# Performance work log

Hardware: AMD Instinct MI355X
Metric: run time of the kernel (lower is better)

Reference implementation:

```python
import jax, jax.numpy as jnp
import numpy as np

N = 50000      # nodes
E = 625000     # directed edges
F_IN, H1, H2, OUT = 128, 128, 64, 50


def setup_inputs() -> dict:
    key = jax.random.key(0)
    ks = jax.random.split(key, 5)
    x = jax.random.normal(ks[0], (N, F_IN), dtype=jnp.float32)
    edge_index = jax.random.randint(ks[1], (2, E), 0, N, dtype=jnp.int64)
    W1 = jax.random.normal(ks[2], (F_IN, H1), dtype=jnp.float32) * 0.05
    b1 = jnp.zeros((H1,), jnp.float32)
    W2 = jax.random.normal(ks[3], (H1, H2), dtype=jnp.float32) * 0.05
    b2 = jnp.zeros((H2,), jnp.float32)
    Wh = jax.random.normal(ks[4], (H2, OUT), dtype=jnp.float32) * 0.05
    bh = jnp.zeros((OUT,), jnp.float32)
    return {"x": x, "edge_index": edge_index, "W1": W1, "b1": b1,
            "W2": W2, "b2": b2, "Wh": Wh, "bh": bh}


def _gcn_conv(h, W, b, src, dst, dinv, n):
    # h' = D^{-1/2} A_hat D^{-1/2} (h W) + b, A_hat includes self-loops
    h = h @ W                                   # [n, out]
    coef = (dinv[src] * dinv[dst])[:, None]      # [e, 1]
    agg = jax.ops.segment_sum(h[src] * coef, dst, num_segments=n)
    return agg + b


def reference(x, edge_index, W1, b1, W2, b2, Wh, bh):
    n = x.shape[0]
    loops = jnp.arange(n, dtype=edge_index.dtype)
    src = jnp.concatenate([edge_index[0], loops])
    dst = jnp.concatenate([edge_index[1], loops])
    # symmetric GCN normalization: deg over destinations (incl. self-loops)
    deg = jax.ops.segment_sum(jnp.ones(src.shape[0], x.dtype), dst, num_segments=n)
    dinv = jnp.where(deg > 0, jax.lax.rsqrt(deg), 0.0)
    # dropout is a no-op in eval mode (training=False)
    h = _gcn_conv(x, W1, b1, src, dst, dinv, n)
    h = jax.nn.relu(h)
    h = _gcn_conv(h, W2, b2, src, dst, dinv, n)
    h = jax.nn.relu(h)
    return h @ Wh + bh
```

## Files before the change

kernel.cpp:

```cpp
#include <hip/hip_runtime.h>

#define F_IN 128
#define HH1 128
#define HH2 64
#define FOUT 50
#define EB 256
#define NBUCK_MAX 256

typedef __attribute__((ext_vector_type(8))) short short8;
typedef __attribute__((ext_vector_type(4))) short s16x4;
typedef __attribute__((ext_vector_type(4))) float f32x4;

__device__ inline short f2bf(float f) {
    union { float f; unsigned u; } v; v.f = f;
    unsigned r = v.u + 0x7fffu + ((v.u >> 16) & 1u);
    return (short)(r >> 16);
}
__device__ inline float bf2f(short s) {
    union { float f; unsigned u; } v; v.u = ((unsigned)(unsigned short)s) << 16;
    return v.f;
}

__device__ inline int detect64(const unsigned* raw) {
    __shared__ int s_is64;
    if (threadIdx.x == 0) s_is64 = 1;
    __syncthreads();
    if (raw[2 * threadIdx.x + 1] != 0u) atomicAnd(&s_is64, 0);
    __syncthreads();
    return s_is64;
}

__global__ __launch_bounds__(256) void bucket_count(
    const int* __restrict__ raw, int E, int nbuck, int* __restrict__ parthist,
    const float* __restrict__ W1, const float* __restrict__ W2,
    const float* __restrict__ Wh, short* __restrict__ W1t,
    short* __restrict__ W2t, short* __restrict__ Wht) {
    __shared__ int hist[NBUCK_MAX];
    const int tid = threadIdx.x;
    int is64 = detect64((const unsigned*)raw);
    for (int k = tid; k < nbuck; k += 256) hist[k] = 0;
    __syncthreads();
    const int CH = (E + EB - 1) / EB;
    const int e0 = blockIdx.x * CH, e1 = min(E, e0 + CH);
    for (int e = e0 + tid; e < e1; e += 256) {
        int d = is64 ? raw[2 * (long)E + 2 * e] : raw[E + e];
        atomicAdd(&hist[d >> 8], 1);
    }
    __syncthreads();
    for (int k = tid; k < nbuck; k += 256) parthist[blockIdx.x * nbuck + k] = hist[k];
    const int T1 = HH1 * F_IN, T2 = HH2 * HH1, T3 = 64 * HH2;
    int idx = blockIdx.x * 256 + tid;
    if (idx < T1) {
        int c = idx / F_IN, k = idx - c * F_IN;
        W1t[idx] = f2bf(W1[(long)k * HH1 + c]);
    } else if (idx < T1 + T2) {
        int i = idx - T1;
        int c = i / HH1, k = i - c * HH1;
        W2t[i] = f2bf(W2[(long)k * HH2 + c]);
    } else if (idx < T1 + T2 + T3) {
        int i = idx - T1 - T2;
        int c = i / HH2, k = i - c * HH2;
        Wht[i] = f2bf((c < FOUT) ? Wh[(long)k * FOUT + c] : 0.f);
    }
}

__global__ __launch_bounds__(256) void bucket_scan(
    int* __restrict__ parthist, int* __restrict__ bbase, int nbuck, int E) {
    __shared__ int sh[256];
    const int k = threadIdx.x;
    int sum = 0;
    if (k < nbuck)
        for (int b = 0; b < EB; ++b) sum += parthist[b * nbuck + k];
    int v = (k < nbuck) ? sum : 0;
    sh[k] = v;
    __syncthreads();
    for (int off = 1; off < 256; off <<= 1) {
        int t = (k >= off) ? sh[k - off] : 0;
        __syncthreads();
        sh[k] += t;
        __syncthreads();
    }
    int base = sh[k] - v;
    if (k < nbuck) bbase[k] = base;
    if (k == 0) bbase[nbuck] = E;
    if (k < nbuck) {
        int run = base;
        for (int b = 0; b < EB; ++b) {
            int t = parthist[b * nbuck + k];
            parthist[b * nbuck + k] = run;
            run += t;
        }
    }
}

__global__ __launch_bounds__(256) void bucket_scatter(
    const int* __restrict__ raw, int E, int nbuck,
    const int* __restrict__ parthist, int2* __restrict__ tmp) {
    __shared__ int cur[NBUCK_MAX];
    const int tid = threadIdx.x;
    int is64 = detect64((const unsigned*)raw);
    for (int k = tid; k < nbuck; k += 256) cur[k] = parthist[blockIdx.x * nbuck + k];
    __syncthreads();
    const int CH = (E + EB - 1) / EB;
    const int e0 = blockIdx.x * CH, e1 = min(E, e0 + CH);
    for (int e = e0 + tid; e < e1; e += 256) {
        int s, d;
        if (is64) {
            s = raw[2 * e];
            d = raw[2 * (long)E + 2 * e];
        } else {
            s = raw[e];
            d = raw[E + e];
        }
        int pos = atomicAdd(&cur[d >> 8], 1);
        tmp[pos] = make_int2(s, d);
    }
}

__global__ __launch_bounds__(256) void bucket_finalize(
    const int2* __restrict__ tmp, const int* __restrict__ bbase,
    int* __restrict__ rowptr, float* __restrict__ dinv,
    int* __restrict__ csr_src, int n, int nbuck) {
    __shared__ int deg[256];
    __shared__ int cur[256];
    __shared__ int sh[256];
    const int k = blockIdx.x;
    const int tid = threadIdx.x;
    const int b0 = bbase[k], b1 = bbase[k + 1];
    deg[tid] = 0;
    __syncthreads();
    for (int e = b0 + tid; e < b1; e += 256) atomicAdd(&deg[tmp[e].y & 255], 1);
    __syncthreads();
    int v = deg[tid];
    sh[tid] = v;
    __syncthreads();
    for (int off = 1; off < 256; off <<= 1) {
        int t = (tid >= off) ? sh[tid - off] : 0;
        __syncthreads();
        sh[tid] += t;
        __syncthreads();
    }
    int excl = sh[tid] - v;
    cur[tid] = excl;
    int node = (k << 8) + tid;
    if (node < n) {
        rowptr[node] = b0 + excl;
        dinv[node] = rsqrtf((float)v + 1.0f);
    }
    if (k == 0 && tid == 0) rowptr[n] = bbase[nbuck];
    __syncthreads();
    for (int e = b0 + tid; e < b1; e += 256) {
        int2 sd = tmp[e];
        int p = atomicAdd(&cur[sd.y & 255], 1);
        csr_src[b0 + p] = sd.x;
    }
}

template <int K, int NC, bool IN_BF16, bool OUT_F32, bool BIAS>
__global__ __launch_bounds__(256) void mfma_gemm(const void* __restrict__ Xv,
                                                 const short* __restrict__ Wt,
                                                 const float* __restrict__ bias,
                                                 void* __restrict__ Yv, int M, int NCOUT) {
    const int tid = threadIdx.x;
    const int wave = tid >> 6;
    const int lane = tid & 63;
    const int l15 = lane & 15;
    const int kg = lane >> 4;
    const int rowbase = blockIdx.x * 64 + wave * 16;
    const int arow = rowbase + l15;
    constexpr int KS = K / 32;

    short8 af[KS];
    if (arow < M) {
        if (IN_BF16) {
            const short* xr = (const short*)Xv + (long)arow * K + kg * 8;
#pragma unroll
            for (int ks = 0; ks < KS; ++ks) af[ks] = *(const short8*)(xr + ks * 32);
        } else {
            const float* xr = (const float*)Xv + (long)arow * K + kg * 8;
#pragma unroll
            for (int ks = 0; ks < KS; ++ks) {
                float4 f0 = *(const float4*)(xr + ks * 32);
                float4 f1 = *(const float4*)(xr + ks * 32 + 4);
                short8 a;
                a[0] = f2bf(f0.x); a[1] = f2bf(f0.y); a[2] = f2bf(f0.z); a[3] = f2bf(f0.w);
                a[4] = f2bf(f1.x); a[5] = f2bf(f1.y); a[6] = f2bf(f1.z); a[7] = f2bf(f1.w);
                af[ks] = a;
            }
        }
    } else {
#pragma unroll
        for (int ks = 0; ks < KS; ++ks) af[ks] = (short8)0;
    }

    const int crowb = rowbase + kg * 4;
#pragma unroll
    for (int ct = 0; ct < NC / 16; ++ct) {
        const int col = ct * 16 + l15;
        const short* wr = Wt + (long)col * K + kg * 8;
        f32x4 acc = {0.f, 0.f, 0.f, 0.f};
#pragma unroll
        for (int ks = 0; ks < KS; ++ks) {
            short8 bf = *(const short8*)(wr + ks * 32);
            acc = __builtin_amdgcn_mfma_f32_16x16x32_bf16(af[ks], bf, acc, 0, 0, 0);
        }
        if (OUT_F32) {
            float* Y = (float*)Yv;
            float bv = BIAS ? bias[col] : 0.f;
#pragma unroll
            for (int j = 0; j < 4; ++j) {
                int r = crowb + j;
                if (r < M && col < NCOUT) Y[(long)r * NCOUT + col] = acc[j] + bv;
            }
        } else {
            short* Y = (short*)Yv;
#pragma unroll
            for (int j = 0; j < 4; ++j) {
                int r = crowb + j;
                if (r < M) Y[(long)r * NC + col] = f2bf(acc[j]);
            }
        }
    }
}

template <int FPL>
__device__ inline void gather2(const short* p0, const short* p1, float c0,
                               float c1, float* acc) {
    if constexpr (FPL == 8) {
        short8 v0 = *(const short8*)p0;
        short8 v1 = *(const short8*)p1;
#pragma unroll
        for (int j = 0; j < 8; ++j) acc[j] = fmaf(c0, bf2f(v0[j]), acc[j]);
#pragma unroll
        for (int j = 0; j < 8; ++j) acc[j] = fmaf(c1, bf2f(v1[j]), acc[j]);
    } else {
        s16x4 v0 = *(const s16x4*)p0;
        s16x4 v1 = *(const s16x4*)p1;
#pragma unroll
        for (int j = 0; j < 4; ++j) acc[j] = fmaf(c0, bf2f(v0[j]), acc[j]);
#pragma unroll
        for (int j = 0; j < 4; ++j) acc[j] = fmaf(c1, bf2f(v1[j]), acc[j]);
    }
}
template <int FPL>
__device__ inline void gather1(const short* p0, float c0, float* acc) {
    if constexpr (FPL == 8) {
        short8 v0 = *(const short8*)p0;
#pragma unroll
        for (int j = 0; j < 8; ++j) acc[j] = fmaf(c0, bf2f(v0[j]), acc[j]);
    } else {
        s16x4 v0 = *(const s16x4*)p0;
#pragma unroll
        for (int j = 0; j < 4; ++j) acc[j] = fmaf(c0, bf2f(v0[j]), acc[j]);
    }
}

template <int FW, bool OUT_F32>
__global__ __launch_bounds__(256) void agg_mm(
    const short* __restrict__ h, const int* __restrict__ rowptr,
    const int* __restrict__ csr_src, const float* __restrict__ dinv,
    const float* __restrict__ bias_pre, const short* __restrict__ Wt,
    const float* __restrict__ bias_post, void* __restrict__ Yv, int n,
    int ncreal) {
    constexpr int FPL = FW / 16;
    constexpr int LDW = FW + 8;
    constexpr int KS = FW / 32;
    __shared__ short tile[16][LDW];
    const int tid = threadIdx.x;
    const int grp = tid >> 4;
    const int l16 = tid & 15;
    const int node = blockIdx.x * 16 + grp;

    float acc[FPL];
#pragma unroll
    for (int j = 0; j < FPL; ++j) acc[j] = 0.f;

    if (node < n) {
        const float di = dinv[node];
#pragma unroll
        for (int j = 0; j < FPL; ++j) acc[j] = bias_pre[l16 * FPL + j];
        gather1<FPL>(h + (long)node * FW + l16 * FPL, di * di, acc);
        int e = rowptr[node];
        const int end = rowptr[node + 1];
        for (; e + 1 < end; e += 2) {
            int s0 = csr_src[e];
            int s1 = csr_src[e + 1];
            float c0 = dinv[s0] * di;
            float c1 = dinv[s1] * di;
            gather2<FPL>(h + (long)s0 * FW + l16 * FPL,
                         h + (long)s1 * FW + l16 * FPL, c0, c1, acc);
        }
        if (e < end) {
            int s0 = csr_src[e];
            gather1<FPL>(h + (long)s0 * FW + l16 * FPL, dinv[s0] * di, acc);
        }
    }
    if constexpr (FPL == 8) {
        short8 o;
#pragma unroll
        for (int j = 0; j < 8; ++j) o[j] = f2bf(fmaxf(acc[j], 0.f));
        *(short8*)&tile[grp][l16 * 8] = o;
    } else {
        s16x4 o;
#pragma unroll
        for (int j = 0; j < 4; ++j) o[j] = f2bf(fmaxf(acc[j], 0.f));
        *(s16x4*)&tile[grp][l16 * 4] = o;
    }
    __syncthreads();

    const int wave = tid >> 6;
    const int lane = tid & 63;
    const int l15 = lane & 15;
    const int kg = lane >> 4;
    const int col = wave * 16 + l15;
    short8 af[KS];
#pragma unroll
    for (int ks = 0; ks < KS; ++ks)
        af[ks] = *(const short8*)&tile[l15][kg * 8 + ks * 32];
    f32x4 c2 = {0.f, 0.f, 0.f, 0.f};
    const short* wr = Wt + (long)col * FW + kg * 8;
#pragma unroll
    for (int ks = 0; ks < KS; ++ks) {
        short8 bfr = *(const short8*)(wr + ks * 32);
        c2 = __builtin_amdgcn_mfma_f32_16x16x32_bf16(af[ks], bfr, c2, 0, 0, 0);
    }
    const int rb = blockIdx.x * 16 + kg * 4;
    if (OUT_F32) {
        float* Y = (float*)Yv;
#pragma unroll
        for (int j = 0; j < 4; ++j) {
            int g = rb + j;
            if (g < n && col < ncreal)
                Y[(long)g * ncreal + col] = c2[j] + bias_post[col];
        }
    } else {
        short* Y = (short*)Yv;
#pragma unroll
        for (int j = 0; j < 4; ++j) {
            int g = rb + j;
            if (g < n) Y[(long)g * 64 + col] = f2bf(c2[j]);
        }
    }
}

static inline size_t al256(size_t x) { return (x + 255) & ~(size_t)255; }

extern "C" void kernel_launch(void* const* d_in, const int* in_sizes, int n_in,
                              void* d_out, int out_size, void* d_ws, size_t ws_size,
                              hipStream_t stream) {
    const float* x    = (const float*)d_in[0];
    const int*   eraw = (const int*)d_in[1];
    const float* W1   = (const float*)d_in[2];
    const float* b1   = (const float*)d_in[3];
    const float* W2   = (const float*)d_in[4];
    const float* b2   = (const float*)d_in[5];
    const float* Wh   = (const float*)d_in[6];
    const float* bh   = (const float*)d_in[7];
    float* out = (float*)d_out;
    const int n = in_sizes[0] / F_IN;
    const int E = in_sizes[1] / 2;
    const int nbuck = (n + 255) >> 8;

    char* p = (char*)d_ws;
    float* dinv     = (float*)p; p += al256((size_t)n * 4);
    int*   rowptr   = (int*)p;   p += al256((size_t)(n + 1) * 4);
    int*   parthist = (int*)p;   p += al256((size_t)EB * nbuck * 4);
    int*   bbase    = (int*)p;   p += al256((size_t)(nbuck + 1) * 4);
    int*   csr_src  = (int*)p;   p += al256((size_t)E * 4);
    short* W1t      = (short*)p; p += al256((size_t)HH1 * F_IN * 2);
    short* W2t      = (short*)p; p += al256((size_t)HH2 * HH1 * 2);
    short* Whtp     = (short*)p; p += al256((size_t)64 * HH2 * 2);
    short* bigA     = (short*)p; p += al256((size_t)n * HH1 * 2);
    short* bigB     = (short*)p;
    int2* tmp   = (int2*)bigA;
    short* h1   = bigA;
    short* h2   = bigB;

    dim3 blk(256);
    bucket_count<<<EB, blk, 0, stream>>>(eraw, E, nbuck, parthist, W1, W2, Wh, W1t, W2t, Whtp);
    bucket_scan<<<1, blk, 0, stream>>>(parthist, bbase, nbuck, E);
    bucket_scatter<<<EB, blk, 0, stream>>>(eraw, E, nbuck, parthist, tmp);
    bucket_finalize<<<nbuck, blk, 0, stream>>>(tmp, bbase, rowptr, dinv, csr_src, n, nbuck);

    mfma_gemm<F_IN, HH1, false, false, false><<<(n + 63) / 64, blk, 0, stream>>>(
        x, W1t, nullptr, h1, n, HH1);
    agg_mm<HH1, false><<<(n + 15) / 16, blk, 0, stream>>>(
        h1, rowptr, csr_src, dinv, b1, W2t, nullptr, h2, n, HH2);
    agg_mm<HH2, true><<<(n + 15) / 16, blk, 0, stream>>>(
        h2, rowptr, csr_src, dinv, b2, Whtp, bh, out, n, FOUT);
}
```

Baseline: 137.7 us.

## Fuse edge bucket scatter with first-layer GEMM and unroll gather by four

Merges the bucket scatter kernel and the layer-1 MFMA GEMM into one launch. The first EB blocks do the scatter and the remaining blocks compute x@W1 into h1. Because the two now run concurrently, tmp gets its own workspace buffer instead of aliasing h1. The aggregation loop also goes from 2 to 4 edges per iteration to raise memory-level parallelism. This removes one launch and lets the independent GEMM overlap the atomic-heavy scatter, at the cost of extra workspace and more registers in the gather loop.

```diff
diff --git a/kernel.cpp b/kernel.cpp
--- a/kernel.cpp
+++ b/kernel.cpp
@@ -93,27 +93,74 @@
     }
 }
 
-__global__ __launch_bounds__(256) void bucket_scatter(
+__global__ __launch_bounds__(256) void scatter_gemm1(
     const int* __restrict__ raw, int E, int nbuck,
-    const int* __restrict__ parthist, int2* __restrict__ tmp) {
-    __shared__ int cur[NBUCK_MAX];
+    const int* __restrict__ parthist, int2* __restrict__ tmp,
+    const float* __restrict__ x, const short* __restrict__ W1t,
+    short* __restrict__ h1, int n) {
     const int tid = threadIdx.x;
-    int is64 = detect64((const unsigned*)raw);
-    for (int k = tid; k < nbuck; k += 256) cur[k] = parthist[blockIdx.x * nbuck + k];
-    __syncthreads();
-    const int CH = (E + EB - 1) / EB;
-    const int e0 = blockIdx.x * CH, e1 = min(E, e0 + CH);
-    for (int e = e0 + tid; e < e1; e += 256) {
-        int s, d;
-        if (is64) {
-            s = raw[2 * e];
-            d = raw[2 * (long)E + 2 * e];
-        } else {
-            s = raw[e];
-            d = raw[E + e];
-        }
-        int pos = atomicAdd(&cur[d >> 8], 1);
-        tmp[pos] = make_int2(s, d);
+    if (blockIdx.x < EB) {
+        __shared__ int cur[NBUCK_MAX];
+        int is64 = detect64((const unsigned*)raw);
+        for (int k = tid; k < nbuck; k += 256) cur[k] = parthist[blockIdx.x * nbuck + k];
+        __syncthreads();
+        const int CH = (E + EB - 1) / EB;
+        const int e0 = blockIdx.x * CH, e1 = min(E, e0 + CH);
+        for (int e = e0 + tid; e < e1; e += 256) {
+            int s, d;
+            if (is64) {
+                s = raw[2 * e];
+                d = raw[2 * (long)E + 2 * e];
+            } else {
+                s = raw[e];
+                d = raw[E + e];
+            }
+            int pos = atomicAdd(&cur[d >> 8], 1);
+            tmp[pos] = make_int2(s, d);
+        }
+        return;
+    }
+    const int bid = blockIdx.x - EB;
+    const int wave = tid >> 6;
+    const int lane = tid & 63;
+    const int l15 = lane & 15;
+    const int kg = lane >> 4;
+    const int rowbase = bid * 64 + wave * 16;
+    const int arow = rowbase + l15;
+    constexpr int KS = F_IN / 32;
+
+    short8 af[KS];
+    if (arow < n) {
+        const float* xr = x + (long)arow * F_IN + kg * 8;
+#pragma unroll
+        for (int ks = 0; ks < KS; ++ks) {
+            float4 f0 = *(const float4*)(xr + ks * 32);
+            float4 f1 = *(const float4*)(xr + ks * 32 + 4);
+            short8 a;
+            a[0] = f2bf(f0.x); a[1] = f2bf(f0.y); a[2] = f2bf(f0.z); a[3] = f2bf(f0.w);
+            a[4] = f2bf(f1.x); a[5] = f2bf(f1.y); a[6] = f2bf(f1.z); a[7] = f2bf(f1.w);
+            af[ks] = a;
+        }
+    } else {
+#pragma unroll
+        for (int ks = 0; ks < KS; ++ks) af[ks] = (short8)0;
+    }
+    const int crowb = rowbase + kg * 4;
+#pragma unroll
+    for (int ct = 0; ct < HH1 / 16; ++ct) {
+        const int col = ct * 16 + l15;
+        const short* wr = W1t + (long)col * F_IN + kg * 8;
+        f32x4 acc = {0.f, 0.f, 0.f, 0.f};
+#pragma unroll
+        for (int ks = 0; ks < KS; ++ks) {
+            short8 bfr = *(const short8*)(wr + ks * 32);
+            acc = __builtin_amdgcn_mfma_f32_16x16x32_bf16(af[ks], bfr, acc, 0, 0, 0);
+        }
+#pragma unroll
+        for (int j = 0; j < 4; ++j) {
+            int r = crowb + j;
+            if (r < n) h1[(long)r * HH1 + col] = f2bf(acc[j]);
+        }
     }
 }
 
@@ -156,92 +203,6 @@
     }
 }
 
-template <int K, int NC, bool IN_BF16, bool OUT_F32, bool BIAS>
-__global__ __launch_bounds__(256) void mfma_gemm(const void* __restrict__ Xv,
-                                                 const short* __restrict__ Wt,
-                                                 const float* __restrict__ bias,
-                                                 void* __restrict__ Yv, int M, int NCOUT) {
-    const int tid = threadIdx.x;
-    const int wave = tid >> 6;
-    const int lane = tid & 63;
-    const int l15 = lane & 15;
-    const int kg = lane >> 4;
-    const int rowbase = blockIdx.x * 64 + wave * 16;
-    const int arow = rowbase + l15;
-    constexpr int KS = K / 32;
-
-    short8 af[KS];
-    if (arow < M) {
-        if (IN_BF16) {
-            const short* xr = (const short*)Xv + (long)arow * K + kg * 8;
-#pragma unroll
-            for (int ks = 0; ks < KS; ++ks) af[ks] = *(const short8*)(xr + ks * 32);
-        } else {
-            const float* xr = (const float*)Xv + (long)arow * K + kg * 8;
-#pragma unroll
-            for (int ks = 0; ks < KS; ++ks) {
-                float4 f0 = *(const float4*)(xr + ks * 32);
-                float4 f1 = *(const float4*)(xr + ks * 32 + 4);
-                short8 a;
-                a[0] = f2bf(f0.x); a[1] = f2bf(f0.y); a[2] = f2bf(f0.z); a[3] = f2bf(f0.w);
-                a[4] = f2bf(f1.x); a[5] = f2bf(f1.y); a[6] = f2bf(f1.z); a[7] = f2bf(f1.w);
-                af[ks] = a;
-            }
-        }
-    } else {
-#pragma unroll
-        for (int ks = 0; ks < KS; ++ks) af[ks] = (short8)0;
-    }
-
-    const int crowb = rowbase + kg * 4;
-#pragma unroll
-    for (int ct = 0; ct < NC / 16; ++ct) {
-        const int col = ct * 16 + l15;
-        const short* wr = Wt + (long)col * K + kg * 8;
-        f32x4 acc = {0.f, 0.f, 0.f, 0.f};
-#pragma unroll
-        for (int ks = 0; ks < KS; ++ks) {
-            short8 bf = *(const short8*)(wr + ks * 32);
-            acc = __builtin_amdgcn_mfma_f32_16x16x32_bf16(af[ks], bf, acc, 0, 0, 0);
-        }
-        if (OUT_F32) {
-            float* Y = (float*)Yv;
-            float bv = BIAS ? bias[col] : 0.f;
-#pragma unroll
-            for (int j = 0; j < 4; ++j) {
-                int r = crowb + j;
-                if (r < M && col < NCOUT) Y[(long)r * NCOUT + col] = acc[j] + bv;
-            }
-        } else {
-            short* Y = (short*)Yv;
-#pragma unroll
-            for (int j = 0; j < 4; ++j) {
-                int r = crowb + j;
-                if (r < M) Y[(long)r * NC + col] = f2bf(acc[j]);
-            }
-        }
-    }
-}
-
-template <int FPL>
-__device__ inline void gather2(const short* p0, const short* p1, float c0,
-                               float c1, float* acc) {
-    if constexpr (FPL == 8) {
-        short8 v0 = *(const short8*)p0;
-        short8 v1 = *(const short8*)p1;
-#pragma unroll
-        for (int j = 0; j < 8; ++j) acc[j] = fmaf(c0, bf2f(v0[j]), acc[j]);
-#pragma unroll
-        for (int j = 0; j < 8; ++j) acc[j] = fmaf(c1, bf2f(v1[j]), acc[j]);
-    } else {
-        s16x4 v0 = *(const s16x4*)p0;
-        s16x4 v1 = *(const s16x4*)p1;
-#pragma unroll
-        for (int j = 0; j < 4; ++j) acc[j] = fmaf(c0, bf2f(v0[j]), acc[j]);
-#pragma unroll
-        for (int j = 0; j < 4; ++j) acc[j] = fmaf(c1, bf2f(v1[j]), acc[j]);
-    }
-}
 template <int FPL>
 __device__ inline void gather1(const short* p0, float c0, float* acc) {
     if constexpr (FPL == 8) {
@@ -282,15 +243,48 @@
         gather1<FPL>(h + (long)node * FW + l16 * FPL, di * di, acc);
         int e = rowptr[node];
         const int end = rowptr[node + 1];
-        for (; e + 1 < end; e += 2) {
+        for (; e + 3 < end; e += 4) {
             int s0 = csr_src[e];
             int s1 = csr_src[e + 1];
+            int s2 = csr_src[e + 2];
+            int s3 = csr_src[e + 3];
+            const short* p0 = h + (long)s0 * FW + l16 * FPL;
+            const short* p1 = h + (long)s1 * FW + l16 * FPL;
+            const short* p2 = h + (long)s2 * FW + l16 * FPL;
+            const short* p3 = h + (long)s3 * FW + l16 * FPL;
             float c0 = dinv[s0] * di;
             float c1 = dinv[s1] * di;
-            gather2<FPL>(h + (long)s0 * FW + l16 * FPL,
-                         h + (long)s1 * FW + l16 * FPL, c0, c1, acc);
-        }
-        if (e < end) {
+            float c2 = dinv[s2] * di;
+            float c3 = dinv[s3] * di;
+            if constexpr (FPL == 8) {
+                short8 v0 = *(const short8*)p0;
+                short8 v1 = *(const short8*)p1;
+                short8 v2 = *(const short8*)p2;
+                short8 v3 = *(const short8*)p3;
+#pragma unroll
+                for (int j = 0; j < 8; ++j) acc[j] = fmaf(c0, bf2f(v0[j]), acc[j]);
+#pragma unroll
+                for (int j = 0; j < 8; ++j) acc[j] = fmaf(c1, bf2f(v1[j]), acc[j]);
+#pragma unroll
+                for (int j = 0; j < 8; ++j) acc[j] = fmaf(c2, bf2f(v2[j]), acc[j]);
+#pragma unroll
+                for (int j = 0; j < 8; ++j) acc[j] = fmaf(c3, bf2f(v3[j]), acc[j]);
+            } else {
+                s16x4 v0 = *(const s16x4*)p0;
+                s16x4 v1 = *(const s16x4*)p1;
+                s16x4 v2 = *(const s16x4*)p2;
+                s16x4 v3 = *(const s16x4*)p3;
+#pragma unroll
+                for (int j = 0; j < 4; ++j) acc[j] = fmaf(c0, bf2f(v0[j]), acc[j]);
+#pragma unroll
+                for (int j = 0; j < 4; ++j) acc[j] = fmaf(c1, bf2f(v1[j]), acc[j]);
+#pragma unroll
+                for (int j = 0; j < 4; ++j) acc[j] = fmaf(c2, bf2f(v2[j]), acc[j]);
+#pragma unroll
+                for (int j = 0; j < 4; ++j) acc[j] = fmaf(c3, bf2f(v3[j]), acc[j]);
+            }
+        }
+        for (; e < end; ++e) {
             int s0 = csr_src[e];
             gather1<FPL>(h + (long)s0 * FW + l16 * FPL, dinv[s0] * di, acc);
         }
@@ -370,20 +364,17 @@
     short* W1t      = (short*)p; p += al256((size_t)HH1 * F_IN * 2);
     short* W2t      = (short*)p; p += al256((size_t)HH2 * HH1 * 2);
     short* Whtp     = (short*)p; p += al256((size_t)64 * HH2 * 2);
-    short* bigA     = (short*)p; p += al256((size_t)n * HH1 * 2);
-    short* bigB     = (short*)p;
-    int2* tmp   = (int2*)bigA;
-    short* h1   = bigA;
-    short* h2   = bigB;
+    int2*  tmp      = (int2*)p;  p += al256((size_t)E * 8);
+    short* h1       = (short*)p; p += al256((size_t)n * HH1 * 2);
+    short* h2       = (short*)p;
 
     dim3 blk(256);
     bucket_count<<<EB, blk, 0, stream>>>(eraw, E, nbuck, parthist, W1, W2, Wh, W1t, W2t, Whtp);
     bucket_scan<<<1, blk, 0, stream>>>(parthist, bbase, nbuck, E);
-    bucket_scatter<<<EB, blk, 0, stream>>>(eraw, E, nbuck, parthist, tmp);
+    scatter_gemm1<<<EB + (n + 63) / 64, blk, 0, stream>>>(
+        eraw, E, nbuck, parthist, tmp, x, W1t, h1, n);
     bucket_finalize<<<nbuck, blk, 0, stream>>>(tmp, bbase, rowptr, dinv, csr_src, n, nbuck);
 
-    mfma_gemm<F_IN, HH1, false, false, false><<<(n + 63) / 64, blk, 0, stream>>>(
-        x, W1t, nullptr, h1, n, HH1);
     agg_mm<HH1, false><<<(n + 15) / 16, blk, 0, stream>>>(
         h1, rowptr, csr_src, dinv, b1, W2t, nullptr, h2, n, HH2);
     agg_mm<HH2, true><<<(n + 15) / 16, blk, 0, stream>>>(
```

New measurement: 121.4 us. 11.8% less time.
